# Optimization experiments

Measured on AMD Instinct MI355X. Metric: run time of the kernel, lower is better.

Reference implementation:

```python
import jax, jax.numpy as jnp
import numpy as np
import math

D_MODEL = 1024
N_HEADS = 16
D_HEAD = D_MODEL // N_HEADS
WINDOW = 256
SCALE = 1.0 / math.sqrt(D_HEAD)


def setup_inputs() -> dict:
    key = jax.random.key(0)
    kx, kqkv, kout = jax.random.split(key, 3)
    x = jax.random.normal(kx, (2, 2048, D_MODEL), dtype=jnp.float32)
    # xavier_uniform for nn.Linear weights (shape [out, in] in torch; store as [in, out] for x @ W)
    lim_qkv = math.sqrt(6.0 / (D_MODEL + 3 * D_MODEL))
    W_qkv = jax.random.uniform(kqkv, (D_MODEL, 3 * D_MODEL), dtype=jnp.float32, minval=-lim_qkv, maxval=lim_qkv)
    lim_out = math.sqrt(6.0 / (D_MODEL + D_MODEL))
    W_out = jax.random.uniform(kout, (D_MODEL, D_MODEL), dtype=jnp.float32, minval=-lim_out, maxval=lim_out)
    return {"x": x, "W_qkv": W_qkv, "W_out": W_out}


def _window_mask(seq_len: int) -> jnp.ndarray:
    # causal + sliding window: position i attends to j with i-WINDOW < j <= i
    i = jnp.arange(seq_len)[:, None]
    j = jnp.arange(seq_len)[None, :]
    allowed = (j <= i) & (j > i - WINDOW)
    return jnp.where(allowed, 0.0, -jnp.inf).astype(jnp.float32)


def reference(x, W_qkv, W_out):
    B, S, _ = x.shape
    qkv = x @ W_qkv                                   # [B, S, 3*D]
    qkv = qkv.reshape(B, S, 3, N_HEADS, D_HEAD)
    qkv = jnp.transpose(qkv, (2, 0, 3, 1, 4))         # [3, B, H, S, Dh]
    q, k, v = qkv[0], qkv[1], qkv[2]
    scores = jnp.einsum('bhsd,bhtd->bhst', q, k) * SCALE
    scores = scores + _window_mask(S)[None, None]
    weights = jax.nn.softmax(scores, axis=-1)
    out = jnp.einsum('bhst,bhtd->bhsd', weights, v)   # [B, H, S, Dh]
    out = jnp.transpose(out, (0, 2, 1, 3)).reshape(B, S, D_MODEL)
    return out @ W_out
```

## Files before the change

kernel.cpp:

```cpp
#include <hip/hip_runtime.h>

typedef unsigned short u16;
typedef unsigned int u32;

#define D_MODEL 1024
#define N_HEADS 16
#define D_HEAD 64
#define WIN 256
#define SEQ 2048
#define BATCH 2
#define NROWS (BATCH*SEQ)

typedef short frag_ab __attribute__((ext_vector_type(8)));
typedef float frag_cd __attribute__((ext_vector_type(4)));
typedef float f32x16 __attribute__((ext_vector_type(16)));
typedef u16 u16x8 __attribute__((ext_vector_type(8)));

__device__ __forceinline__ u16 f2bf(float f) {
    union { float f; u32 u; } x; x.f = f;
    u32 r = x.u + 0x7fffu + ((x.u >> 16) & 1u);
    return (u16)(r >> 16);
}
__device__ __forceinline__ float bf2f(u16 v) {
    union { u32 u; float f; } x; x.u = ((u32)v) << 16; return x.f;
}

__device__ __forceinline__ void load_lds16(const void* g, void* l) {
    __builtin_amdgcn_global_load_lds(
        (const __attribute__((address_space(1))) void*)g,
        (__attribute__((address_space(3))) void*)l, 16, 0, 0);
}

__device__ __forceinline__ void transpose_tile(const float* __restrict__ W, u16* __restrict__ WT,
                                               int K, int N, int n0, int k0,
                                               int scale_rows, float scale) {
    __shared__ float tile[32][33];
    int x = threadIdx.x & 31, y = threadIdx.x >> 5;
#pragma unroll
    for (int r = 0; r < 4; r++)
        tile[y + 8 * r][x] = W[(size_t)(k0 + y + 8 * r) * N + n0 + x];
    __syncthreads();
#pragma unroll
    for (int r = 0; r < 4; r++) {
        int nrow = n0 + y + 8 * r;
        float v = tile[x][y + 8 * r];
        if (nrow < scale_rows) v *= scale;
        WT[(size_t)nrow * K + k0 + x] = f2bf(v);
    }
}

__global__ __launch_bounds__(256) void prep_kernel(const float* __restrict__ x,
                                                   const float* __restrict__ W_qkv,
                                                   const float* __restrict__ W_out,
                                                   u16* __restrict__ xb,
                                                   u16* __restrict__ wqkvT,
                                                   u16* __restrict__ woutT,
                                                   float qscale) {
    const int bid = blockIdx.x;
    if (bid < 4096) {
        int idx = bid * 256 + threadIdx.x;
        float4 v = ((const float4*)x)[idx];
        ushort4 o;
        o.x = f2bf(v.x); o.y = f2bf(v.y); o.z = f2bf(v.z); o.w = f2bf(v.w);
        ((ushort4*)xb)[idx] = o;
    } else if (bid < 4096 + 3072) {
        int t = bid - 4096;
        transpose_tile(W_qkv, wqkvT, D_MODEL, 3 * D_MODEL, (t % 96) * 32, (t / 96) * 32,
                       D_MODEL, qscale);
    } else {
        int t = bid - 7168;
        transpose_tile(W_out, woutT, D_MODEL, D_MODEL, (t % 32) * 32, (t / 32) * 32, 0, 1.0f);
    }
}

template <bool BF16_OUT, int BM>
__global__ __launch_bounds__(256, 4) void gemm_bk64(const u16* __restrict__ A,
                                                    const u16* __restrict__ BT,
                                                    void* __restrict__ C,
                                                    int M, int N, int K) {
    constexpr int MT = BM / 64;
    __shared__ union SMem {
        struct { u16 As[BM * 64]; u16 Bs[128 * 64]; } s;
        u16 cs[BF16_OUT ? BM * 136 : 1];
    } sm;
    const int tid = threadIdx.x;
    const int m0 = blockIdx.y * BM, n0 = blockIdx.x * 128;
    const int wave = tid >> 6, lane = tid & 63;
    const int wm = (wave >> 1) * (BM / 2), wn = (wave & 1) * 64;
    const int l32 = lane & 31, kh = lane >> 5;

    f32x16 acc[MT][2] = {};

    const int r0 = tid >> 3;
    const int w  = (tid & 7) ^ (r0 & 7);
    const u16* aP = A  + (size_t)(m0 + r0) * K + w * 8;
    const u16* bP = BT + (size_t)(n0 + r0) * K + w * 8;

    for (int k0 = 0; k0 < K; k0 += 64) {
        __syncthreads();
#pragma unroll
        for (int u = 0; u < BM / 32; u++)
            load_lds16(aP + (size_t)(32 * u) * K + k0, &sm.s.As[(tid + 256 * u) * 8]);
#pragma unroll
        for (int u = 0; u < 4; u++)
            load_lds16(bP + (size_t)(32 * u) * K + k0, &sm.s.Bs[(tid + 256 * u) * 8]);
        __syncthreads();

#pragma unroll
        for (int kk = 0; kk < 4; kk++) {
            const int csel = ((kk * 2 + kh) ^ (l32 & 7)) * 8;
            frag_ab af[MT], bf[2];
#pragma unroll
            for (int t = 0; t < MT; t++)
                af[t] = *(const frag_ab*)&sm.s.As[(wm + t * 32 + l32) * 64 + csel];
#pragma unroll
            for (int t = 0; t < 2; t++)
                bf[t] = *(const frag_ab*)&sm.s.Bs[(wn + t * 32 + l32) * 64 + csel];
#pragma unroll
            for (int mt = 0; mt < MT; mt++)
#pragma unroll
                for (int nt = 0; nt < 2; nt++)
                    acc[mt][nt] = __builtin_amdgcn_mfma_f32_32x32x16_bf16(af[mt], bf[nt], acc[mt][nt], 0, 0, 0);
        }
    }

    if constexpr (BF16_OUT) {
        __syncthreads();
#pragma unroll
        for (int mt = 0; mt < MT; mt++)
#pragma unroll
            for (int nt = 0; nt < 2; nt++) {
                int col = wn + nt * 32 + l32;
#pragma unroll
                for (int reg = 0; reg < 16; reg++) {
                    int row = wm + mt * 32 + (reg & 3) + 8 * (reg >> 2) + 4 * kh;
                    sm.cs[row * 136 + col] = f2bf(acc[mt][nt][reg]);
                }
            }
        __syncthreads();
        const int cc = tid & 15, rb = tid >> 4;
#pragma unroll
        for (int i = 0; i < BM / 16; i++) {
            int row = rb + 16 * i;
            u16x8 vv = *(const u16x8*)&sm.cs[row * 136 + cc * 8];
            *(u16x8*)((u16*)C + (size_t)(m0 + row) * N + n0 + cc * 8) = vv;
        }
    } else {
#pragma unroll
        for (int mt = 0; mt < MT; mt++)
#pragma unroll
            for (int nt = 0; nt < 2; nt++) {
                int col = n0 + wn + nt * 32 + l32;
#pragma unroll
                for (int reg = 0; reg < 16; reg++) {
                    int row = m0 + wm + mt * 32 + (reg & 3) + 8 * (reg >> 2) + 4 * kh;
                    ((float*)C)[(size_t)row * N + col] = acc[mt][nt][reg];
                }
            }
    }
}

__global__ __launch_bounds__(256) void attn_kernel(const u16* __restrict__ qkv, u16* __restrict__ out) {
    __shared__ u16 Ks[2][64 * 64];
    __shared__ u16 Vt[64 * 72];
    __shared__ u16 ps[4][16 * 72];

    const int tid = threadIdx.x;
    const int wave = tid >> 6, lane = tid & 63;
    const int quad = lane >> 4, c16 = lane & 15;

    const int qc = blockIdx.x & 31;
    const int h  = (blockIdx.x >> 5) & 15;
    const int b  = blockIdx.x >> 9;
    const int q0 = qc * 64;
    const int qw0 = q0 + wave * 16;

    frag_ab qf[2];
    {
        const u16* qrow = qkv + (size_t)(b * SEQ + qw0 + c16) * 3072 + h * 64;
        qf[0] = *(const frag_ab*)(qrow + quad * 8);
        qf[1] = *(const frag_ab*)(qrow + 32 + quad * 8);
    }

    float m_r[4], l_r[4];
    frag_cd acc[4] = {};

    const int ntiles = qc < 4 ? qc + 1 : 5;

    const int krow = wave * 16 + (lane >> 3);
    const int kchunk = (lane & 7) ^ (lane >> 3);
    const int vj2 = (tid & 31) * 2, vd8 = tid >> 5;

    const u16* kbase = qkv + (size_t)(b * SEQ + krow) * 3072 + 1024 + h * 64 + kchunk * 8;
    const u16* vbase = qkv + (size_t)(b * SEQ + vj2) * 3072 + 2048 + h * 64 + vd8 * 8;

    u16x8 va, vb;
    {
        const u16* g = kbase + (size_t)q0 * 3072;
        load_lds16(g,            &Ks[0][krow * 64 + (lane & 7) * 8]);
        load_lds16(g + 8 * 3072, &Ks[0][(krow + 8) * 64 + (lane & 7) * 8]);
        const u16* gv = vbase + (size_t)q0 * 3072;
        va = *(const u16x8*)gv;
        vb = *(const u16x8*)(gv + 3072);
#pragma unroll
        for (int dd = 0; dd < 8; dd++)
            *(u32*)&Vt[(vd8 * 8 + dd) * 72 + vj2] = (u32)va[dd] | ((u32)vb[dd] << 16);
    }

    for (int t = 0; t < ntiles; t++) {
        const int cur = t & 1, nxt = cur ^ 1;
        const int j0 = q0 - 64 * t;
        __syncthreads();
        const bool pre = (t + 1 < ntiles);
        if (pre) {
            const u16* g = kbase + (size_t)(j0 - 64) * 3072;
            load_lds16(g,            &Ks[nxt][krow * 64 + (lane & 7) * 8]);
            load_lds16(g + 8 * 3072, &Ks[nxt][(krow + 8) * 64 + (lane & 7) * 8]);
            const u16* gv = vbase + (size_t)(j0 - 64) * 3072;
            va = *(const u16x8*)gv;
            vb = *(const u16x8*)(gv + 3072);
        }

        frag_cd s[4] = {};
#pragma unroll
        for (int kb = 0; kb < 4; kb++) {
            frag_ab kf0 = *(const frag_ab*)&Ks[cur][(kb * 16 + c16) * 64 + ((quad    ) ^ (c16 & 7)) * 8];
            frag_ab kf1 = *(const frag_ab*)&Ks[cur][(kb * 16 + c16) * 64 + ((4 + quad) ^ (c16 & 7)) * 8];
            s[kb] = __builtin_amdgcn_mfma_f32_16x16x32_bf16(qf[0], kf0, s[kb], 0, 0, 0);
            s[kb] = __builtin_amdgcn_mfma_f32_16x16x32_bf16(qf[1], kf1, s[kb], 0, 0, 0);
        }

        if (t == 0) {
#pragma unroll
            for (int reg = 0; reg < 4; reg++) {
                const int i = qw0 + quad * 4 + reg;
#pragma unroll
                for (int kb = 0; kb < 4; kb++)
                    if (q0 + kb * 16 + c16 > i) s[kb][reg] = -1e30f;
            }
        } else if (t == 4) {
#pragma unroll
            for (int reg = 0; reg < 4; reg++) {
                const int i = qw0 + quad * 4 + reg;
#pragma unroll
                for (int kb = 0; kb < 4; kb++)
                    if (j0 + kb * 16 + c16 + WIN <= i) s[kb][reg] = -1e30f;
            }
        }

        float mt_[4];
#pragma unroll
        for (int reg = 0; reg < 4; reg++)
            mt_[reg] = fmaxf(fmaxf(s[0][reg], s[1][reg]), fmaxf(s[2][reg], s[3][reg]));
#pragma unroll
        for (int off = 1; off < 16; off <<= 1)
#pragma unroll
            for (int reg = 0; reg < 4; reg++) mt_[reg] = fmaxf(mt_[reg], __shfl_xor(mt_[reg], off));

        float alpha[4];
        if (t == 0) {
#pragma unroll
            for (int reg = 0; reg < 4; reg++) m_r[reg] = mt_[reg];
        } else {
#pragma unroll
            for (int reg = 0; reg < 4; reg++) {
                float mn = fmaxf(m_r[reg], mt_[reg]);
                alpha[reg] = __builtin_amdgcn_exp2f(m_r[reg] - mn);
                m_r[reg] = mn;
            }
        }

        float rs[4] = {0.f, 0.f, 0.f, 0.f};
#pragma unroll
        for (int kb = 0; kb < 4; kb++)
#pragma unroll
            for (int reg = 0; reg < 4; reg++) {
                float p = __builtin_amdgcn_exp2f(s[kb][reg] - m_r[reg]);
                union { float f; u32 u; } pu; pu.f = p;
                ps[wave][(quad * 4 + reg) * 72 + kb * 16 + c16] = (u16)(pu.u >> 16);
                rs[reg] += p;
            }
#pragma unroll
        for (int off = 1; off < 16; off <<= 1)
#pragma unroll
            for (int reg = 0; reg < 4; reg++) rs[reg] += __shfl_xor(rs[reg], off);

        if (t == 0) {
#pragma unroll
            for (int reg = 0; reg < 4; reg++) l_r[reg] = rs[reg];
        } else {
#pragma unroll
            for (int reg = 0; reg < 4; reg++) l_r[reg] = l_r[reg] * alpha[reg] + rs[reg];
#pragma unroll
            for (int dblk = 0; dblk < 4; dblk++)
#pragma unroll
                for (int reg = 0; reg < 4; reg++) acc[dblk][reg] *= alpha[reg];
        }

#pragma unroll
        for (int js = 0; js < 2; js++) {
            frag_ab pf = *(const frag_ab*)&ps[wave][c16 * 72 + js * 32 + quad * 8];
#pragma unroll
            for (int dblk = 0; dblk < 4; dblk++) {
                frag_ab vf = *(const frag_ab*)&Vt[(dblk * 16 + c16) * 72 + js * 32 + quad * 8];
                acc[dblk] = __builtin_amdgcn_mfma_f32_16x16x32_bf16(pf, vf, acc[dblk], 0, 0, 0);
            }
        }

        if (pre) {
            __syncthreads();
#pragma unroll
            for (int dd = 0; dd < 8; dd++)
                *(u32*)&Vt[(vd8 * 8 + dd) * 72 + vj2] = (u32)va[dd] | ((u32)vb[dd] << 16);
        }
    }

    float inv[4];
#pragma unroll
    for (int reg = 0; reg < 4; reg++) inv[reg] = 1.f / l_r[reg];
#pragma unroll
    for (int dblk = 0; dblk < 4; dblk++)
#pragma unroll
        for (int reg = 0; reg < 4; reg++)
            out[(size_t)(b * SEQ + qw0 + quad * 4 + reg) * 1024 + h * 64 + dblk * 16 + c16] =
                f2bf(acc[dblk][reg] * inv[reg]);
}

extern "C" void kernel_launch(void* const* d_in, const int* in_sizes, int n_in,
                              void* d_out, int out_size, void* d_ws, size_t ws_size,
                              hipStream_t stream) {
    const float* x     = (const float*)d_in[0];
    const float* W_qkv = (const float*)d_in[1];
    const float* W_out = (const float*)d_in[2];
    float* out = (float*)d_out;

    char* ws = (char*)d_ws;
    u16* xb    = (u16*)(ws);
    u16* wqkvT = (u16*)(ws + 8388608);
    u16* woutT = (u16*)(ws + 14680064);
    u16* qkvb  = (u16*)(ws + 16777216);
    u16* attnb = (u16*)(ws + 41943040);

    const float QSCALE = 0.125f * 1.4426950408889634f;

    prep_kernel<<<8192, 256, 0, stream>>>(x, W_qkv, W_out, xb, wqkvT, woutT, QSCALE);
    gemm_bk64<true, 128><<<dim3(3 * D_MODEL / 128, NROWS / 128), 256, 0, stream>>>(
        xb, wqkvT, qkvb, NROWS, 3 * D_MODEL, D_MODEL);
    attn_kernel<<<BATCH * N_HEADS * (SEQ / 64), 256, 0, stream>>>(qkvb, attnb);
    gemm_bk64<false, 64><<<dim3(D_MODEL / 128, NROWS / 64), 256, 0, stream>>>(
        attnb, woutT, out, NROWS, D_MODEL, D_MODEL);
}
```

Before: 154.6 us.

## Register-prefetch QKV GEMM, move W_out transpose into attention launch, swap grid order

Adds a new QKV projection GEMM that prefetches the next K-slice into registers while MFMAs run on the current LDS tile, replacing the direct global-to-LDS loads. The W_out transpose moves out of the prep kernel and runs as extra blocks of the attention launch, so it overlaps with attention work and shortens prep. Both GEMMs now put the M tiles on grid x, which changes the block scheduling order and how weights are reused in cache. The costs are higher register pressure (launch bounds lowered to 3 blocks per SM) and transpose blocks mixed into the attention grid.

Result: no change. 154.4 us (-0.1%).

```diff
diff --git a/kernel.cpp b/kernel.cpp
--- a/kernel.cpp
+++ b/kernel.cpp
@@ -33,8 +33,7 @@
 
 __device__ __forceinline__ void transpose_tile(const float* __restrict__ W, u16* __restrict__ WT,
                                                int K, int N, int n0, int k0,
-                                               int scale_rows, float scale) {
-    __shared__ float tile[32][33];
+                                               int scale_rows, float scale, float (*tile)[33]) {
     int x = threadIdx.x & 31, y = threadIdx.x >> 5;
 #pragma unroll
     for (int r = 0; r < 4; r++)
@@ -51,11 +50,10 @@
 
 __global__ __launch_bounds__(256) void prep_kernel(const float* __restrict__ x,
                                                    const float* __restrict__ W_qkv,
-                                                   const float* __restrict__ W_out,
                                                    u16* __restrict__ xb,
                                                    u16* __restrict__ wqkvT,
-                                                   u16* __restrict__ woutT,
                                                    float qscale) {
+    __shared__ float tile[32][33];
     const int bid = blockIdx.x;
     if (bid < 4096) {
         int idx = bid * 256 + threadIdx.x;
@@ -63,47 +61,125 @@
         ushort4 o;
         o.x = f2bf(v.x); o.y = f2bf(v.y); o.z = f2bf(v.z); o.w = f2bf(v.w);
         ((ushort4*)xb)[idx] = o;
-    } else if (bid < 4096 + 3072) {
+    } else {
         int t = bid - 4096;
         transpose_tile(W_qkv, wqkvT, D_MODEL, 3 * D_MODEL, (t % 96) * 32, (t / 96) * 32,
-                       D_MODEL, qscale);
-    } else {
-        int t = bid - 7168;
-        transpose_tile(W_out, woutT, D_MODEL, D_MODEL, (t % 32) * 32, (t / 32) * 32, 0, 1.0f);
-    }
-}
-
-template <bool BF16_OUT, int BM>
-__global__ __launch_bounds__(256, 4) void gemm_bk64(const u16* __restrict__ A,
+                       D_MODEL, qscale, tile);
+    }
+}
+
+__global__ __launch_bounds__(256, 3) void gemm_pipe(const u16* __restrict__ A,
                                                     const u16* __restrict__ BT,
-                                                    void* __restrict__ C,
+                                                    u16* __restrict__ C,
                                                     int M, int N, int K) {
-    constexpr int MT = BM / 64;
     __shared__ union SMem {
-        struct { u16 As[BM * 64]; u16 Bs[128 * 64]; } s;
-        u16 cs[BF16_OUT ? BM * 136 : 1];
+        struct { u16 As[128 * 64]; u16 Bs[128 * 64]; } s;
+        u16 cs[128 * 136];
     } sm;
     const int tid = threadIdx.x;
-    const int m0 = blockIdx.y * BM, n0 = blockIdx.x * 128;
+    const int m0 = blockIdx.x * 128, n0 = blockIdx.y * 128;
     const int wave = tid >> 6, lane = tid & 63;
-    const int wm = (wave >> 1) * (BM / 2), wn = (wave & 1) * 64;
+    const int wm = (wave >> 1) * 64, wn = (wave & 1) * 64;
     const int l32 = lane & 31, kh = lane >> 5;
 
-    f32x16 acc[MT][2] = {};
+    f32x16 acc[2][2] = {};
 
     const int r0 = tid >> 3;
     const int w  = (tid & 7) ^ (r0 & 7);
     const u16* aP = A  + (size_t)(m0 + r0) * K + w * 8;
     const u16* bP = BT + (size_t)(n0 + r0) * K + w * 8;
 
+    u16x8 ar[4], br[4];
+#pragma unroll
+    for (int u = 0; u < 4; u++) {
+        ar[u] = *(const u16x8*)(aP + (size_t)(32 * u) * K);
+        br[u] = *(const u16x8*)(bP + (size_t)(32 * u) * K);
+    }
+
     for (int k0 = 0; k0 < K; k0 += 64) {
         __syncthreads();
 #pragma unroll
+        for (int u = 0; u < 4; u++) {
+            *(u16x8*)&sm.s.As[(tid + 256 * u) * 8] = ar[u];
+            *(u16x8*)&sm.s.Bs[(tid + 256 * u) * 8] = br[u];
+        }
+        __syncthreads();
+
+        if (k0 + 64 < K) {
+#pragma unroll
+            for (int u = 0; u < 4; u++) {
+                ar[u] = *(const u16x8*)(aP + (size_t)(32 * u) * K + k0 + 64);
+                br[u] = *(const u16x8*)(bP + (size_t)(32 * u) * K + k0 + 64);
+            }
+        }
+
+#pragma unroll
+        for (int kk = 0; kk < 4; kk++) {
+            const int csel = ((kk * 2 + kh) ^ (l32 & 7)) * 8;
+            frag_ab af[2], bf[2];
+#pragma unroll
+            for (int t = 0; t < 2; t++) {
+                af[t] = *(const frag_ab*)&sm.s.As[(wm + t * 32 + l32) * 64 + csel];
+                bf[t] = *(const frag_ab*)&sm.s.Bs[(wn + t * 32 + l32) * 64 + csel];
+            }
+#pragma unroll
+            for (int mt = 0; mt < 2; mt++)
+#pragma unroll
+                for (int nt = 0; nt < 2; nt++)
+                    acc[mt][nt] = __builtin_amdgcn_mfma_f32_32x32x16_bf16(af[mt], bf[nt], acc[mt][nt], 0, 0, 0);
+        }
+    }
+
+    __syncthreads();
+#pragma unroll
+    for (int mt = 0; mt < 2; mt++)
+#pragma unroll
+        for (int nt = 0; nt < 2; nt++) {
+            int col = wn + nt * 32 + l32;
+#pragma unroll
+            for (int reg = 0; reg < 16; reg++) {
+                int row = wm + mt * 32 + (reg & 3) + 8 * (reg >> 2) + 4 * kh;
+                sm.cs[row * 136 + col] = f2bf(acc[mt][nt][reg]);
+            }
+        }
+    __syncthreads();
+    const int cc = tid & 15, rb = tid >> 4;
+#pragma unroll
+    for (int i = 0; i < 8; i++) {
+        int row = rb + 16 * i;
+        u16x8 vv = *(const u16x8*)&sm.cs[row * 136 + cc * 8];
+        *(u16x8*)(C + (size_t)(m0 + row) * N + n0 + cc * 8) = vv;
+    }
+}
+
+template <int BM>
+__global__ __launch_bounds__(256, 4) void gemm_bk64(const u16* __restrict__ A,
+                                                    const u16* __restrict__ BT,
+                                                    float* __restrict__ C,
+                                                    int M, int N, int K) {
+    constexpr int MT = BM / 64;
+    __shared__ struct { u16 As[BM * 64]; u16 Bs[128 * 64]; } sm;
+    const int tid = threadIdx.x;
+    const int m0 = blockIdx.x * BM, n0 = blockIdx.y * 128;
+    const int wave = tid >> 6, lane = tid & 63;
+    const int wm = (wave >> 1) * (BM / 2), wn = (wave & 1) * 64;
+    const int l32 = lane & 31, kh = lane >> 5;
+
+    f32x16 acc[MT][2] = {};
+
+    const int r0 = tid >> 3;
+    const int w  = (tid & 7) ^ (r0 & 7);
+    const u16* aP = A  + (size_t)(m0 + r0) * K + w * 8;
+    const u16* bP = BT + (size_t)(n0 + r0) * K + w * 8;
+
+    for (int k0 = 0; k0 < K; k0 += 64) {
+        __syncthreads();
+#pragma unroll
         for (int u = 0; u < BM / 32; u++)
-            load_lds16(aP + (size_t)(32 * u) * K + k0, &sm.s.As[(tid + 256 * u) * 8]);
+            load_lds16(aP + (size_t)(32 * u) * K + k0, &sm.As[(tid + 256 * u) * 8]);
 #pragma unroll
         for (int u = 0; u < 4; u++)
-            load_lds16(bP + (size_t)(32 * u) * K + k0, &sm.s.Bs[(tid + 256 * u) * 8]);
+            load_lds16(bP + (size_t)(32 * u) * K + k0, &sm.Bs[(tid + 256 * u) * 8]);
         __syncthreads();
 
 #pragma unroll
@@ -112,10 +188,10 @@
             frag_ab af[MT], bf[2];
 #pragma unroll
             for (int t = 0; t < MT; t++)
-                af[t] = *(const frag_ab*)&sm.s.As[(wm + t * 32 + l32) * 64 + csel];
+                af[t] = *(const frag_ab*)&sm.As[(wm + t * 32 + l32) * 64 + csel];
 #pragma unroll
             for (int t = 0; t < 2; t++)
-                bf[t] = *(const frag_ab*)&sm.s.Bs[(wn + t * 32 + l32) * 64 + csel];
+                bf[t] = *(const frag_ab*)&sm.Bs[(wn + t * 32 + l32) * 64 + csel];
 #pragma unroll
             for (int mt = 0; mt < MT; mt++)
 #pragma unroll
@@ -124,46 +200,32 @@
         }
     }
 
-    if constexpr (BF16_OUT) {
-        __syncthreads();
-#pragma unroll
-        for (int mt = 0; mt < MT; mt++)
-#pragma unroll
-            for (int nt = 0; nt < 2; nt++) {
-                int col = wn + nt * 32 + l32;
-#pragma unroll
-                for (int reg = 0; reg < 16; reg++) {
-                    int row = wm + mt * 32 + (reg & 3) + 8 * (reg >> 2) + 4 * kh;
-                    sm.cs[row * 136 + col] = f2bf(acc[mt][nt][reg]);
-                }
-            }
-        __syncthreads();
-        const int cc = tid & 15, rb = tid >> 4;
-#pragma unroll
-        for (int i = 0; i < BM / 16; i++) {
-            int row = rb + 16 * i;
-            u16x8 vv = *(const u16x8*)&sm.cs[row * 136 + cc * 8];
-            *(u16x8*)((u16*)C + (size_t)(m0 + row) * N + n0 + cc * 8) = vv;
-        }
-    } else {
-#pragma unroll
-        for (int mt = 0; mt < MT; mt++)
-#pragma unroll
-            for (int nt = 0; nt < 2; nt++) {
-                int col = n0 + wn + nt * 32 + l32;
-#pragma unroll
-                for (int reg = 0; reg < 16; reg++) {
-                    int row = m0 + wm + mt * 32 + (reg & 3) + 8 * (reg >> 2) + 4 * kh;
-                    ((float*)C)[(size_t)row * N + col] = acc[mt][nt][reg];
-                }
-            }
-    }
-}
-
-__global__ __launch_bounds__(256) void attn_kernel(const u16* __restrict__ qkv, u16* __restrict__ out) {
+#pragma unroll
+    for (int mt = 0; mt < MT; mt++)
+#pragma unroll
+        for (int nt = 0; nt < 2; nt++) {
+            int col = n0 + wn + nt * 32 + l32;
+#pragma unroll
+            for (int reg = 0; reg < 16; reg++) {
+                int row = m0 + wm + mt * 32 + (reg & 3) + 8 * (reg >> 2) + 4 * kh;
+                C[(size_t)row * N + col] = acc[mt][nt][reg];
+            }
+        }
+}
+
+__global__ __launch_bounds__(256) void attn_kernel(const u16* __restrict__ qkv, u16* __restrict__ out,
+                                                   const float* __restrict__ W_out,
+                                                   u16* __restrict__ woutT) {
     __shared__ u16 Ks[2][64 * 64];
     __shared__ u16 Vt[64 * 72];
     __shared__ u16 ps[4][16 * 72];
+
+    if (blockIdx.x >= 1024) {
+        int t = blockIdx.x - 1024;
+        transpose_tile(W_out, woutT, D_MODEL, D_MODEL, (t & 31) * 32, (t >> 5) * 32,
+                       0, 1.0f, (float(*)[33])&Ks[0][0]);
+        return;
+    }
 
     const int tid = threadIdx.x;
     const int wave = tid >> 6, lane = tid & 63;
@@ -343,10 +405,10 @@
 
     const float QSCALE = 0.125f * 1.4426950408889634f;
 
-    prep_kernel<<<8192, 256, 0, stream>>>(x, W_qkv, W_out, xb, wqkvT, woutT, QSCALE);
-    gemm_bk64<true, 128><<<dim3(3 * D_MODEL / 128, NROWS / 128), 256, 0, stream>>>(
+    prep_kernel<<<7168, 256, 0, stream>>>(x, W_qkv, xb, wqkvT, QSCALE);
+    gemm_pipe<<<dim3(NROWS / 128, 3 * D_MODEL / 128), 256, 0, stream>>>(
         xb, wqkvT, qkvb, NROWS, 3 * D_MODEL, D_MODEL);
-    attn_kernel<<<BATCH * N_HEADS * (SEQ / 64), 256, 0, stream>>>(qkvb, attnb);
-    gemm_bk64<false, 64><<<dim3(D_MODEL / 128, NROWS / 64), 256, 0, stream>>>(
+    attn_kernel<<<2048, 256, 0, stream>>>(qkvb, attnb, W_out, woutT);
+    gemm_bk64<64><<<dim3(NROWS / 64, D_MODEL / 128), 256, 0, stream>>>(
         attnb, woutT, out, NROWS, D_MODEL, D_MODEL);
 }
```

## Fuse prep, QKV GEMM, attention and output GEMM into one cooperative persistent kernel

Applied to the files above, without the earlier changes.

Replaces the four separate launches (prep, QKV GEMM, attention, output GEMM) with a single cooperative kernel. Persistent blocks loop over each phase's tiles and separate the phases with grid-wide syncs; all phases share one LDS union. The aim is to remove per-launch overhead and the idle gaps between kernels. In exchange it adds grid-sync cost and forces every phase to use the same register budget under launch_bounds(256,4), which could cost the attention phase occupancy or cause spills.

Result: slower. 398.0 us (+157.5%).

```diff
diff --git a/kernel.cpp b/kernel.cpp
--- a/kernel.cpp
+++ b/kernel.cpp
@@ -1,4 +1,7 @@
 #include <hip/hip_runtime.h>
+#include <hip/hip_cooperative_groups.h>
+
+namespace cg = cooperative_groups;
 
 typedef unsigned short u16;
 typedef unsigned int u32;
@@ -21,9 +24,6 @@
     u32 r = x.u + 0x7fffu + ((x.u >> 16) & 1u);
     return (u16)(r >> 16);
 }
-__device__ __forceinline__ float bf2f(u16 v) {
-    union { u32 u; float f; } x; x.u = ((u32)v) << 16; return x.f;
-}
 
 __device__ __forceinline__ void load_lds16(const void* g, void* l) {
     __builtin_amdgcn_global_load_lds(
@@ -31,10 +31,16 @@
         (__attribute__((address_space(3))) void*)l, 16, 0, 0);
 }
 
+union Smem {
+    float tile[32][33];
+    struct { u16 As[128 * 64]; u16 Bs[128 * 64]; } g;
+    u16 cs[128 * 136];
+    struct { u16 Ks[2][64 * 64]; u16 Vt[64 * 72]; u16 ps[4][16 * 72]; } a;
+};
+
 __device__ __forceinline__ void transpose_tile(const float* __restrict__ W, u16* __restrict__ WT,
                                                int K, int N, int n0, int k0,
-                                               int scale_rows, float scale) {
-    __shared__ float tile[32][33];
+                                               int scale_rows, float scale, float (*tile)[33]) {
     int x = threadIdx.x & 31, y = threadIdx.x >> 5;
 #pragma unroll
     for (int r = 0; r < 4; r++)
@@ -49,42 +55,34 @@
     }
 }
 
-__global__ __launch_bounds__(256) void prep_kernel(const float* __restrict__ x,
-                                                   const float* __restrict__ W_qkv,
-                                                   const float* __restrict__ W_out,
-                                                   u16* __restrict__ xb,
-                                                   u16* __restrict__ wqkvT,
-                                                   u16* __restrict__ woutT,
-                                                   float qscale) {
-    const int bid = blockIdx.x;
-    if (bid < 4096) {
-        int idx = bid * 256 + threadIdx.x;
+__device__ __forceinline__ void prep_unit(u32 u, const float* __restrict__ x,
+                                          const float* __restrict__ W_qkv,
+                                          const float* __restrict__ W_out,
+                                          u16* __restrict__ xb, u16* __restrict__ wqkvT,
+                                          u16* __restrict__ woutT, float qscale, Smem& sm) {
+    if (u < 4096) {
+        int idx = u * 256 + threadIdx.x;
         float4 v = ((const float4*)x)[idx];
         ushort4 o;
         o.x = f2bf(v.x); o.y = f2bf(v.y); o.z = f2bf(v.z); o.w = f2bf(v.w);
         ((ushort4*)xb)[idx] = o;
-    } else if (bid < 4096 + 3072) {
-        int t = bid - 4096;
+    } else if (u < 7168) {
+        int t = u - 4096;
         transpose_tile(W_qkv, wqkvT, D_MODEL, 3 * D_MODEL, (t % 96) * 32, (t / 96) * 32,
-                       D_MODEL, qscale);
+                       D_MODEL, qscale, sm.tile);
     } else {
-        int t = bid - 7168;
-        transpose_tile(W_out, woutT, D_MODEL, D_MODEL, (t % 32) * 32, (t / 32) * 32, 0, 1.0f);
+        int t = u - 7168;
+        transpose_tile(W_out, woutT, D_MODEL, D_MODEL, (t & 31) * 32, (t >> 5) * 32,
+                       0, 1.0f, sm.tile);
     }
 }
 
 template <bool BF16_OUT, int BM>
-__global__ __launch_bounds__(256, 4) void gemm_bk64(const u16* __restrict__ A,
-                                                    const u16* __restrict__ BT,
-                                                    void* __restrict__ C,
-                                                    int M, int N, int K) {
+__device__ __forceinline__ void gemm_tile(const u16* __restrict__ A, const u16* __restrict__ BT,
+                                          void* __restrict__ C, int N, int K,
+                                          int m0, int n0, Smem& sm) {
     constexpr int MT = BM / 64;
-    __shared__ union SMem {
-        struct { u16 As[BM * 64]; u16 Bs[128 * 64]; } s;
-        u16 cs[BF16_OUT ? BM * 136 : 1];
-    } sm;
     const int tid = threadIdx.x;
-    const int m0 = blockIdx.y * BM, n0 = blockIdx.x * 128;
     const int wave = tid >> 6, lane = tid & 63;
     const int wm = (wave >> 1) * (BM / 2), wn = (wave & 1) * 64;
     const int l32 = lane & 31, kh = lane >> 5;
@@ -100,10 +98,10 @@
         __syncthreads();
 #pragma unroll
         for (int u = 0; u < BM / 32; u++)
-            load_lds16(aP + (size_t)(32 * u) * K + k0, &sm.s.As[(tid + 256 * u) * 8]);
+            load_lds16(aP + (size_t)(32 * u) * K + k0, &sm.g.As[(tid + 256 * u) * 8]);
 #pragma unroll
         for (int u = 0; u < 4; u++)
-            load_lds16(bP + (size_t)(32 * u) * K + k0, &sm.s.Bs[(tid + 256 * u) * 8]);
+            load_lds16(bP + (size_t)(32 * u) * K + k0, &sm.g.Bs[(tid + 256 * u) * 8]);
         __syncthreads();
 
 #pragma unroll
@@ -112,10 +110,10 @@
             frag_ab af[MT], bf[2];
 #pragma unroll
             for (int t = 0; t < MT; t++)
-                af[t] = *(const frag_ab*)&sm.s.As[(wm + t * 32 + l32) * 64 + csel];
+                af[t] = *(const frag_ab*)&sm.g.As[(wm + t * 32 + l32) * 64 + csel];
 #pragma unroll
             for (int t = 0; t < 2; t++)
-                bf[t] = *(const frag_ab*)&sm.s.Bs[(wn + t * 32 + l32) * 64 + csel];
+                bf[t] = *(const frag_ab*)&sm.g.Bs[(wn + t * 32 + l32) * 64 + csel];
 #pragma unroll
             for (int mt = 0; mt < MT; mt++)
 #pragma unroll
@@ -160,18 +158,15 @@
     }
 }
 
-__global__ __launch_bounds__(256) void attn_kernel(const u16* __restrict__ qkv, u16* __restrict__ out) {
-    __shared__ u16 Ks[2][64 * 64];
-    __shared__ u16 Vt[64 * 72];
-    __shared__ u16 ps[4][16 * 72];
-
+__device__ __forceinline__ void attn_tile(u32 tile_id, const u16* __restrict__ qkv,
+                                          u16* __restrict__ out, Smem& sm) {
     const int tid = threadIdx.x;
     const int wave = tid >> 6, lane = tid & 63;
     const int quad = lane >> 4, c16 = lane & 15;
 
-    const int qc = blockIdx.x & 31;
-    const int h  = (blockIdx.x >> 5) & 15;
-    const int b  = blockIdx.x >> 9;
+    const int qc = tile_id & 31;
+    const int h  = (tile_id >> 5) & 15;
+    const int b  = tile_id >> 9;
     const int q0 = qc * 64;
     const int qw0 = q0 + wave * 16;
 
@@ -197,14 +192,14 @@
     u16x8 va, vb;
     {
         const u16* g = kbase + (size_t)q0 * 3072;
-        load_lds16(g,            &Ks[0][krow * 64 + (lane & 7) * 8]);
-        load_lds16(g + 8 * 3072, &Ks[0][(krow + 8) * 64 + (lane & 7) * 8]);
+        load_lds16(g,            &sm.a.Ks[0][krow * 64 + (lane & 7) * 8]);
+        load_lds16(g + 8 * 3072, &sm.a.Ks[0][(krow + 8) * 64 + (lane & 7) * 8]);
         const u16* gv = vbase + (size_t)q0 * 3072;
         va = *(const u16x8*)gv;
         vb = *(const u16x8*)(gv + 3072);
 #pragma unroll
         for (int dd = 0; dd < 8; dd++)
-            *(u32*)&Vt[(vd8 * 8 + dd) * 72 + vj2] = (u32)va[dd] | ((u32)vb[dd] << 16);
+            *(u32*)&sm.a.Vt[(vd8 * 8 + dd) * 72 + vj2] = (u32)va[dd] | ((u32)vb[dd] << 16);
     }
 
     for (int t = 0; t < ntiles; t++) {
@@ -214,8 +209,8 @@
         const bool pre = (t + 1 < ntiles);
         if (pre) {
             const u16* g = kbase + (size_t)(j0 - 64) * 3072;
-            load_lds16(g,            &Ks[nxt][krow * 64 + (lane & 7) * 8]);
-            load_lds16(g + 8 * 3072, &Ks[nxt][(krow + 8) * 64 + (lane & 7) * 8]);
+            load_lds16(g,            &sm.a.Ks[nxt][krow * 64 + (lane & 7) * 8]);
+            load_lds16(g + 8 * 3072, &sm.a.Ks[nxt][(krow + 8) * 64 + (lane & 7) * 8]);
             const u16* gv = vbase + (size_t)(j0 - 64) * 3072;
             va = *(const u16x8*)gv;
             vb = *(const u16x8*)(gv + 3072);
@@ -224,8 +219,8 @@
         frag_cd s[4] = {};
 #pragma unroll
         for (int kb = 0; kb < 4; kb++) {
-            frag_ab kf0 = *(const frag_ab*)&Ks[cur][(kb * 16 + c16) * 64 + ((quad    ) ^ (c16 & 7)) * 8];
-            frag_ab kf1 = *(const frag_ab*)&Ks[cur][(kb * 16 + c16) * 64 + ((4 + quad) ^ (c16 & 7)) * 8];
+            frag_ab kf0 = *(const frag_ab*)&sm.a.Ks[cur][(kb * 16 + c16) * 64 + ((quad    ) ^ (c16 & 7)) * 8];
+            frag_ab kf1 = *(const frag_ab*)&sm.a.Ks[cur][(kb * 16 + c16) * 64 + ((4 + quad) ^ (c16 & 7)) * 8];
             s[kb] = __builtin_amdgcn_mfma_f32_16x16x32_bf16(qf[0], kf0, s[kb], 0, 0, 0);
             s[kb] = __builtin_amdgcn_mfma_f32_16x16x32_bf16(qf[1], kf1, s[kb], 0, 0, 0);
         }
@@ -277,7 +272,7 @@
             for (int reg = 0; reg < 4; reg++) {
                 float p = __builtin_amdgcn_exp2f(s[kb][reg] - m_r[reg]);
                 union { float f; u32 u; } pu; pu.f = p;
-                ps[wave][(quad * 4 + reg) * 72 + kb * 16 + c16] = (u16)(pu.u >> 16);
+                sm.a.ps[wave][(quad * 4 + reg) * 72 + kb * 16 + c16] = (u16)(pu.u >> 16);
                 rs[reg] += p;
             }
 #pragma unroll
@@ -299,10 +294,10 @@
 
 #pragma unroll
         for (int js = 0; js < 2; js++) {
-            frag_ab pf = *(const frag_ab*)&ps[wave][c16 * 72 + js * 32 + quad * 8];
+            frag_ab pf = *(const frag_ab*)&sm.a.ps[wave][c16 * 72 + js * 32 + quad * 8];
 #pragma unroll
             for (int dblk = 0; dblk < 4; dblk++) {
-                frag_ab vf = *(const frag_ab*)&Vt[(dblk * 16 + c16) * 72 + js * 32 + quad * 8];
+                frag_ab vf = *(const frag_ab*)&sm.a.Vt[(dblk * 16 + c16) * 72 + js * 32 + quad * 8];
                 acc[dblk] = __builtin_amdgcn_mfma_f32_16x16x32_bf16(pf, vf, acc[dblk], 0, 0, 0);
             }
         }
@@ -311,7 +306,7 @@
             __syncthreads();
 #pragma unroll
             for (int dd = 0; dd < 8; dd++)
-                *(u32*)&Vt[(vd8 * 8 + dd) * 72 + vj2] = (u32)va[dd] | ((u32)vb[dd] << 16);
+                *(u32*)&sm.a.Vt[(vd8 * 8 + dd) * 72 + vj2] = (u32)va[dd] | ((u32)vb[dd] << 16);
         }
     }
 
@@ -324,6 +319,32 @@
         for (int reg = 0; reg < 4; reg++)
             out[(size_t)(b * SEQ + qw0 + quad * 4 + reg) * 1024 + h * 64 + dblk * 16 + c16] =
                 f2bf(acc[dblk][reg] * inv[reg]);
+}
+
+__global__ __launch_bounds__(256, 4) void mega_kernel(
+    const float* __restrict__ x, const float* __restrict__ W_qkv, const float* __restrict__ W_out,
+    u16* __restrict__ xb, u16* __restrict__ wqkvT, u16* __restrict__ woutT,
+    u16* __restrict__ qkvb, u16* __restrict__ attnb, float* __restrict__ out, float qscale) {
+    __shared__ Smem sm;
+    cg::grid_group grid = cg::this_grid();
+
+    for (u32 u = blockIdx.x; u < 8192; u += gridDim.x) {
+        prep_unit(u, x, W_qkv, W_out, xb, wqkvT, woutT, qscale, sm);
+        __syncthreads();
+    }
+    grid.sync();
+    for (u32 t = blockIdx.x; t < 768; t += gridDim.x)
+        gemm_tile<true, 128>(xb, wqkvT, qkvb, 3 * D_MODEL, D_MODEL,
+                             (int)(t & 31) * 128, (int)(t >> 5) * 128, sm);
+    grid.sync();
+    for (u32 t = blockIdx.x; t < 1024; t += gridDim.x) {
+        __syncthreads();
+        attn_tile(t, qkvb, attnb, sm);
+    }
+    grid.sync();
+    for (u32 t = blockIdx.x; t < 512; t += gridDim.x)
+        gemm_tile<false, 64>(attnb, woutT, out, D_MODEL, D_MODEL,
+                             (int)(t & 63) * 64, (int)(t >> 6) * 128, sm);
 }
 
 extern "C" void kernel_launch(void* const* d_in, const int* in_sizes, int n_in,
@@ -341,12 +362,15 @@
     u16* qkvb  = (u16*)(ws + 16777216);
     u16* attnb = (u16*)(ws + 41943040);
 
-    const float QSCALE = 0.125f * 1.4426950408889634f;
-
-    prep_kernel<<<8192, 256, 0, stream>>>(x, W_qkv, W_out, xb, wqkvT, woutT, QSCALE);
-    gemm_bk64<true, 128><<<dim3(3 * D_MODEL / 128, NROWS / 128), 256, 0, stream>>>(
-        xb, wqkvT, qkvb, NROWS, 3 * D_MODEL, D_MODEL);
-    attn_kernel<<<BATCH * N_HEADS * (SEQ / 64), 256, 0, stream>>>(qkvb, attnb);
-    gemm_bk64<false, 64><<<dim3(D_MODEL / 128, NROWS / 64), 256, 0, stream>>>(
-        attnb, woutT, out, NROWS, D_MODEL, D_MODEL);
-}
+    float qscale = 0.125f * 1.4426950408889634f;
+
+    int occ = 0;
+    hipOccupancyMaxActiveBlocksPerMultiprocessor(&occ, mega_kernel, 256, 0);
+    if (occ < 1) occ = 1;
+    int nblk = occ * 256;
+    if (nblk > 1024) nblk = 1024;
+
+    void* args[] = { (void*)&x, (void*)&W_qkv, (void*)&W_out, (void*)&xb, (void*)&wqkvT,
+                     (void*)&woutT, (void*)&qkvb, (void*)&attnb, (void*)&out, (void*)&qscale };
+    hipLaunchCooperativeKernel(mega_kernel, dim3(nblk), dim3(256), args, 0, stream);
+}
```

## Swizzle GEMM tiles per XCD, reorder attention blocks, move W_out transpose

Applied to the files above, without the earlier changes.

GEMM blocks now use a 1D grid remapped so each XCD (blockIdx mod 8) owns a contiguous set of N columns and walks all M tiles, to improve L2 reuse of the weight panels. Attention block indexing is reordered so consecutive blocks cover different batch-heads for the same query chunk. The W_out transpose moves from the prep kernel into extra blocks of the attention launch, reusing its shared memory. This aims to cut L2 misses and shorten prep, at the cost of a more complex mapping and a heavier tail on the attention grid.

Result: no change. 151.6 us (-1.9%).

```diff
diff --git a/kernel.cpp b/kernel.cpp
--- a/kernel.cpp
+++ b/kernel.cpp
@@ -21,9 +21,6 @@
     u32 r = x.u + 0x7fffu + ((x.u >> 16) & 1u);
     return (u16)(r >> 16);
 }
-__device__ __forceinline__ float bf2f(u16 v) {
-    union { u32 u; float f; } x; x.u = ((u32)v) << 16; return x.f;
-}
 
 __device__ __forceinline__ void load_lds16(const void* g, void* l) {
     __builtin_amdgcn_global_load_lds(
@@ -33,8 +30,7 @@
 
 __device__ __forceinline__ void transpose_tile(const float* __restrict__ W, u16* __restrict__ WT,
                                                int K, int N, int n0, int k0,
-                                               int scale_rows, float scale) {
-    __shared__ float tile[32][33];
+                                               int scale_rows, float scale, float (*tile)[33]) {
     int x = threadIdx.x & 31, y = threadIdx.x >> 5;
 #pragma unroll
     for (int r = 0; r < 4; r++)
@@ -51,11 +47,10 @@
 
 __global__ __launch_bounds__(256) void prep_kernel(const float* __restrict__ x,
                                                    const float* __restrict__ W_qkv,
-                                                   const float* __restrict__ W_out,
                                                    u16* __restrict__ xb,
                                                    u16* __restrict__ wqkvT,
-                                                   u16* __restrict__ woutT,
                                                    float qscale) {
+    __shared__ float tile[32][33];
     const int bid = blockIdx.x;
     if (bid < 4096) {
         int idx = bid * 256 + threadIdx.x;
@@ -63,17 +58,14 @@
         ushort4 o;
         o.x = f2bf(v.x); o.y = f2bf(v.y); o.z = f2bf(v.z); o.w = f2bf(v.w);
         ((ushort4*)xb)[idx] = o;
-    } else if (bid < 4096 + 3072) {
+    } else {
         int t = bid - 4096;
         transpose_tile(W_qkv, wqkvT, D_MODEL, 3 * D_MODEL, (t % 96) * 32, (t / 96) * 32,
-                       D_MODEL, qscale);
-    } else {
-        int t = bid - 7168;
-        transpose_tile(W_out, woutT, D_MODEL, D_MODEL, (t % 32) * 32, (t / 32) * 32, 0, 1.0f);
-    }
-}
-
-template <bool BF16_OUT, int BM>
+                       D_MODEL, qscale, tile);
+    }
+}
+
+template <bool BF16_OUT, int BM, int MB, int NPER>
 __global__ __launch_bounds__(256, 4) void gemm_bk64(const u16* __restrict__ A,
                                                     const u16* __restrict__ BT,
                                                     void* __restrict__ C,
@@ -84,7 +76,9 @@
         u16 cs[BF16_OUT ? BM * 136 : 1];
     } sm;
     const int tid = threadIdx.x;
-    const int m0 = blockIdx.y * BM, n0 = blockIdx.x * 128;
+    const int xcd = blockIdx.x & 7, sblk = blockIdx.x >> 3;
+    const int m0 = (sblk % MB) * BM;
+    const int n0 = (xcd * NPER + sblk / MB) * 128;
     const int wave = tid >> 6, lane = tid & 63;
     const int wm = (wave >> 1) * (BM / 2), wn = (wave & 1) * 64;
     const int l32 = lane & 31, kh = lane >> 5;
@@ -160,18 +154,28 @@
     }
 }
 
-__global__ __launch_bounds__(256) void attn_kernel(const u16* __restrict__ qkv, u16* __restrict__ out) {
+__global__ __launch_bounds__(256) void attn_kernel(const u16* __restrict__ qkv, u16* __restrict__ out,
+                                                   const float* __restrict__ W_out,
+                                                   u16* __restrict__ woutT) {
     __shared__ u16 Ks[2][64 * 64];
     __shared__ u16 Vt[64 * 72];
     __shared__ u16 ps[4][16 * 72];
 
+    if (blockIdx.x >= 1024) {
+        int t = blockIdx.x - 1024;
+        transpose_tile(W_out, woutT, D_MODEL, D_MODEL, (t & 31) * 32, (t >> 5) * 32,
+                       0, 1.0f, (float(*)[33])&Ks[0][0]);
+        return;
+    }
+
     const int tid = threadIdx.x;
     const int wave = tid >> 6, lane = tid & 63;
     const int quad = lane >> 4, c16 = lane & 15;
 
-    const int qc = blockIdx.x & 31;
-    const int h  = (blockIdx.x >> 5) & 15;
-    const int b  = blockIdx.x >> 9;
+    const int bh = blockIdx.x & 31;
+    const int qc = blockIdx.x >> 5;
+    const int h  = bh & 15;
+    const int b  = bh >> 4;
     const int q0 = qc * 64;
     const int qw0 = q0 + wave * 16;
 
@@ -343,10 +347,10 @@
 
     const float QSCALE = 0.125f * 1.4426950408889634f;
 
-    prep_kernel<<<8192, 256, 0, stream>>>(x, W_qkv, W_out, xb, wqkvT, woutT, QSCALE);
-    gemm_bk64<true, 128><<<dim3(3 * D_MODEL / 128, NROWS / 128), 256, 0, stream>>>(
+    prep_kernel<<<7168, 256, 0, stream>>>(x, W_qkv, xb, wqkvT, QSCALE);
+    gemm_bk64<true, 128, 32, 3><<<768, 256, 0, stream>>>(
         xb, wqkvT, qkvb, NROWS, 3 * D_MODEL, D_MODEL);
-    attn_kernel<<<BATCH * N_HEADS * (SEQ / 64), 256, 0, stream>>>(qkvb, attnb);
-    gemm_bk64<false, 64><<<dim3(D_MODEL / 128, NROWS / 64), 256, 0, stream>>>(
+    attn_kernel<<<2048, 256, 0, stream>>>(qkvb, attnb, W_out, woutT);
+    gemm_bk64<false, 64, 64, 1><<<512, 256, 0, stream>>>(
         attnb, woutT, out, NROWS, D_MODEL, D_MODEL);
 }
```
